# Kernel optimization log

Hardware: AMD Instinct MI355X
Metric: run time of the kernel (lower is better)

The kernel has to match this reference:

```python
import jax, jax.numpy as jnp
import numpy as np
from jax import lax

B, S, D, H, K = 2, 2048, 1024, 16, 3  # batch, seq, embed, heads, conv kernel
DEPTH = D // H


def silu(x):
    return x * jax.nn.sigmoid(x)


def sep_conv1d(x, dw, pw, b):
    """Keras SeparableConv1D, padding='same', activation=silu.
    x: [B,S,C]; dw: [K,1,C] depthwise kernel; pw: [C,F] pointwise; b: [F]."""
    C = x.shape[-1]
    y = lax.conv_general_dilated(
        x, dw, window_strides=(1,), padding='SAME',
        dimension_numbers=('NWC', 'WIO', 'NWC'), feature_group_count=C)
    y = jnp.einsum('bsc,cf->bsf', y, pw) + b
    return silu(y)


def setup_inputs() -> dict:
    key = jax.random.key(0)
    ks = jax.random.split(key, 20)
    sc = 1.0 / np.sqrt(D)
    inp = {
        'v': jax.random.normal(ks[0], (B, S, D), jnp.float32),
        'k': jax.random.normal(ks[1], (B, S, D), jnp.float32),
        'q': jax.random.normal(ks[2], (B, S, D), jnp.float32),
        'mask': jax.random.randint(ks[3], (B, 1, 1, S), 0, 2, jnp.int32),
        # Dense wq/wk/wv (SiLU)
        'wq_w': jax.random.normal(ks[4], (D, D), jnp.float32) * sc,
        'wq_b': jnp.zeros((D,), jnp.float32),
        'wk_w': jax.random.normal(ks[5], (D, D), jnp.float32) * sc,
        'wk_b': jnp.zeros((D,), jnp.float32),
        'wv_w': jax.random.normal(ks[6], (D, D), jnp.float32) * sc,
        'wv_b': jnp.zeros((D,), jnp.float32),
        # SeparableConv1D params (depthwise [K,1,D], pointwise [D,D], bias [D])
        'dwq': jax.random.normal(ks[7], (K, 1, D), jnp.float32) * 0.1,
        'pwq': jax.random.normal(ks[8], (D, D), jnp.float32) * sc,
        'bq': jnp.zeros((D,), jnp.float32),
        'dwk': jax.random.normal(ks[9], (K, 1, D), jnp.float32) * 0.1,
        'pwk': jax.random.normal(ks[10], (D, D), jnp.float32) * sc,
        'bk': jnp.zeros((D,), jnp.float32),
        'dwv': jax.random.normal(ks[11], (K, 1, D), jnp.float32) * 0.1,
        'pwv': jax.random.normal(ks[12], (D, D), jnp.float32) * sc,
        'bv': jnp.zeros((D,), jnp.float32),
        # output Dense (SiLU)
        'wo_w': jax.random.normal(ks[13], (D, D), jnp.float32) * sc,
        'wo_b': jnp.zeros((D,), jnp.float32),
    }
    return inp


def reference(v, k, q, mask, wq_w, wq_b, wk_w, wk_b, wv_w, wv_b,
              dwq, pwq, bq, dwk, pwk, bk, dwv, pwv, bv, wo_w, wo_b):
    # Dense projections with SiLU
    qp = silu(q @ wq_w + wq_b)
    kp = silu(k @ wk_w + wk_b)
    vp = silu(v @ wv_w + wv_b)
    # SeparableConv1D enhancements (SiLU)
    qc = sep_conv1d(qp, dwq, pwq, bq)
    kc = sep_conv1d(kp, dwk, pwk, bk)
    vc = sep_conv1d(vp, dwv, pwv, bv)
    # split heads -> [B,H,S,depth]
    def split(x):
        return x.reshape(B, S, H, DEPTH).transpose(0, 2, 1, 3)
    qh, kh, vh = split(qc), split(kc), split(vc)
    # scaled dot-product attention with additive mask penalty
    logits = jnp.einsum('bhqd,bhkd->bhqk', qh, kh) / jnp.sqrt(jnp.float32(DEPTH))
    logits = logits + mask.astype(jnp.float32) * -1e9
    attn = jax.nn.softmax(logits, axis=-1)
    out = jnp.einsum('bhqk,bhkd->bhqd', attn, vh)
    out = out.transpose(0, 2, 1, 3).reshape(B, S, D)
    return silu(out @ wo_w + wo_b)
```

## Files before the change

kernel.cpp:

```cpp
#include <hip/hip_runtime.h>
#include <hip/hip_fp16.h>
#include <math.h>

#define BB 2
#define SS 2048
#define DD 1024
#define HH 16
#define MTOT (BB*SS)

typedef _Float16 f16;
typedef _Float16 f16x4 __attribute__((ext_vector_type(4)));
typedef _Float16 f16x8 __attribute__((ext_vector_type(8)));
typedef float    f32x4 __attribute__((ext_vector_type(4)));

#define KSCALE 0.1803368801111204f

__device__ __forceinline__ float silu_f(float x) {
    return x / (1.0f + __expf(-x));
}

__device__ __forceinline__ void gload16(void* lds, const void* g) {
    __builtin_amdgcn_global_load_lds(
        (const __attribute__((address_space(1))) unsigned*)g,
        (__attribute__((address_space(3))) unsigned*)lds, 16, 0, 0);
}

__global__ __launch_bounds__(256) void prep(
    const float* __restrict__ q, const float* __restrict__ k, const float* __restrict__ v,
    f16* __restrict__ x0, f16* __restrict__ x1, f16* __restrict__ x2,
    const float* __restrict__ w0, const float* __restrict__ w1, const float* __restrict__ w2,
    const float* __restrict__ w3, const float* __restrict__ w4, const float* __restrict__ w5,
    const float* __restrict__ w6, f16* __restrict__ wt,
    const int* __restrict__ mask, int* __restrict__ uidx, int* __restrict__ ucnt)
{
    __shared__ float ts[64][65];
    const int gid = blockIdx.x;
    const int t = threadIdx.x;

    if (gid < 6144) {
        const int z = gid >> 11;
        const float* src = z == 0 ? q : z == 1 ? k : v;
        f16* dst = z == 0 ? x0 : z == 1 ? x1 : x2;
        const size_t i8 = ((size_t)(gid & 2047) * 256 + t) * 8;
        const float4 a = *(const float4*)(src + i8);
        const float4 b = *(const float4*)(src + i8 + 4);
        f16x8 h = {(f16)a.x,(f16)a.y,(f16)a.z,(f16)a.w,(f16)b.x,(f16)b.y,(f16)b.z,(f16)b.w};
        *(f16x8*)(dst + i8) = h;
    } else if (gid < 7936) {
        const int w = gid - 6144;
        const int z = w >> 8;
        const int rem = w & 255;
        const int bn = (rem & 15) << 6, bk = (rem >> 4) << 6;
        const float* src;
        switch (z) {
            case 0: src = w0; break; case 1: src = w1; break;
            case 2: src = w2; break; case 3: src = w3; break;
            case 4: src = w4; break; case 5: src = w5; break;
            default: src = w6; break;
        }
        f16* dst = wt + ((size_t)z << 20);
        #pragma unroll
        for (int i = 0; i < 4; ++i) {
            const int fid = t + (i << 8);
            const int r = fid >> 4, c4 = (fid & 15) << 2;
            const float4 v4 = *(const float4*)(src + (size_t)(bk + r) * 1024 + bn + c4);
            ts[r][c4 + 0] = v4.x; ts[r][c4 + 1] = v4.y;
            ts[r][c4 + 2] = v4.z; ts[r][c4 + 3] = v4.w;
        }
        __syncthreads();
        #pragma unroll
        for (int i = 0; i < 4; ++i) {
            const int fid = t + (i << 8);
            const int nr = fid >> 4, k4 = (fid & 15) << 2;
            f16x4 h = { (f16)ts[k4 + 0][nr], (f16)ts[k4 + 1][nr],
                        (f16)ts[k4 + 2][nr], (f16)ts[k4 + 3][nr] };
            *(f16x4*)(dst + (size_t)(bn + nr) * 1024 + bk + k4) = h;
        }
    } else {
        int* ps = (int*)ts;
        const int b = gid - 7936;
        int f[8]; int cnt = 0;
        const int base = b * SS + t * 8;
        #pragma unroll
        for (int j = 0; j < 8; ++j) { f[j] = (mask[base + j] == 0); cnt += f[j]; }
        ps[t] = cnt;
        __syncthreads();
        for (int off = 1; off < 256; off <<= 1) {
            const int pv = (t >= off) ? ps[t - off] : 0;
            __syncthreads();
            ps[t] += pv;
            __syncthreads();
        }
        int pos = ps[t] - cnt;
        #pragma unroll
        for (int j = 0; j < 8; ++j)
            if (f[j]) uidx[b * SS + pos++] = t * 8 + j;
        const int total = ps[255];
        const int pad = (total + 63) & ~63;
        for (int j = total + t; j < pad; j += 256) uidx[b * SS + j] = 0;
        if (t == 0) { ucnt[b * 2] = total; ucnt[b * 2 + 1] = pad; }
    }
}

__global__ __launch_bounds__(256) void dwconv3g(
    const f16* __restrict__ p0, const f16* __restrict__ p1, const f16* __restrict__ p2,
    const float* __restrict__ w0, const float* __restrict__ w1, const float* __restrict__ w2,
    f16* __restrict__ o0, f16* __restrict__ o1, f16* __restrict__ o2)
{
    const int z = blockIdx.y;
    const f16* x = z == 0 ? p0 : z == 1 ? p1 : p2;
    const float* dw = z == 0 ? w0 : z == 1 ? w1 : w2;
    f16* y = z == 0 ? o0 : z == 1 ? o1 : o2;
    const size_t i8 = ((size_t)blockIdx.x * 256 + threadIdx.x) * 8;
    const int c = (int)(i8 % DD);
    const int s = (int)((i8 / DD) % SS);
    const f16x8 xc = *(const f16x8*)(x + i8);
    float acc[8];
    #pragma unroll
    for (int j = 0; j < 8; ++j) acc[j] = (float)xc[j] * dw[DD + c + j];
    if (s > 0) {
        const f16x8 xm = *(const f16x8*)(x + i8 - DD);
        #pragma unroll
        for (int j = 0; j < 8; ++j) acc[j] = fmaf((float)xm[j], dw[c + j], acc[j]);
    }
    if (s < SS - 1) {
        const f16x8 xp = *(const f16x8*)(x + i8 + DD);
        #pragma unroll
        for (int j = 0; j < 8; ++j) acc[j] = fmaf((float)xp[j], dw[2 * DD + c + j], acc[j]);
    }
    f16x8 o;
    #pragma unroll
    for (int j = 0; j < 8; ++j) o[j] = (f16)acc[j];
    *(f16x8*)(y + i8) = o;
}

struct GArg { const f16* A; const f16* W; const float* b; void* C; float scale; };

template<int OUTF32>
__global__ __launch_bounds__(256) void gemm_f16(GArg g0, GArg g1, GArg g2)
{
    __shared__ f16 As[128 * 64];
    __shared__ f16 Bs[128 * 64];

    const GArg ga = blockIdx.z == 0 ? g0 : blockIdx.z == 1 ? g1 : g2;
    const int t = threadIdx.x, l = t & 63, wv = t >> 6;
    const int lr = l & 15, lg = l >> 4;
    const int wr = wv >> 1, wc = wv & 1;

    const int bid = blockIdx.y * 8 + blockIdx.x;
    const int sw = (bid & 7) * 32 + (bid >> 3);
    const int brow = (sw >> 3) << 7, bcol = (sw & 7) << 7;

    const int srow = l >> 3;
    const int schk = (l & 7) ^ (l >> 3);
    const f16* Abase = ga.A + (size_t)(brow + wv * 32 + srow) * 1024 + schk * 8;
    const f16* Bbase = ga.W + (size_t)(bcol + wv * 32 + srow) * 1024 + schk * 8;

    f32x4 acc[4][4];
    #pragma unroll
    for (int m = 0; m < 4; ++m)
        #pragma unroll
        for (int n = 0; n < 4; ++n) acc[m][n] = (f32x4){0.f, 0.f, 0.f, 0.f};

    for (int kt = 0; kt < 16; ++kt) {
        const int k0 = kt << 6;
        #pragma unroll
        for (int j = 0; j < 4; ++j) {
            gload16(As + (wv * 4 + j) * 512, Abase + (size_t)j * 8 * 1024 + k0);
            gload16(Bs + (wv * 4 + j) * 512, Bbase + (size_t)j * 8 * 1024 + k0);
        }
        __syncthreads();

        #pragma unroll
        for (int kk = 0; kk < 2; ++kk) {
            f16x8 af[4], bf[4];
            #pragma unroll
            for (int m = 0; m < 4; ++m) {
                const int row = (wr << 6) + (m << 4) + lr;
                const int off = row * 128 + ((((kk << 6) | (lg << 4))) ^ ((lr & 7) << 4));
                af[m] = *(const f16x8*)((const char*)As + off);
            }
            #pragma unroll
            for (int n = 0; n < 4; ++n) {
                const int row = (wc << 6) + (n << 4) + lr;
                const int off = row * 128 + ((((kk << 6) | (lg << 4))) ^ ((lr & 7) << 4));
                bf[n] = *(const f16x8*)((const char*)Bs + off);
            }
            #pragma unroll
            for (int m = 0; m < 4; ++m)
                #pragma unroll
                for (int n = 0; n < 4; ++n)
                    acc[m][n] = __builtin_amdgcn_mfma_f32_16x16x32_f16(af[m], bf[n], acc[m][n], 0, 0, 0);
        }
        __syncthreads();
    }

    float bv[4];
    #pragma unroll
    for (int n = 0; n < 4; ++n) bv[n] = ga.b[bcol + (wc << 6) + (n << 4) + lr];
    #pragma unroll
    for (int m = 0; m < 4; ++m)
        #pragma unroll
        for (int n = 0; n < 4; ++n)
            #pragma unroll
            for (int i = 0; i < 4; ++i) {
                const int row = brow + (wr << 6) + (m << 4) + (lg << 2) + i;
                const int col = bcol + (wc << 6) + (n << 4) + lr;
                const float o = silu_f(acc[m][n][i] + bv[n]) * ga.scale;
                if (OUTF32) ((float*)ga.C)[(size_t)row * 1024 + col] = o;
                else        ((f16*)ga.C)[(size_t)row * 1024 + col] = (f16)o;
            }
}

__global__ __launch_bounds__(512) void attn_f16(
    const f16* __restrict__ Q, const f16* __restrict__ Kf,
    const f16* __restrict__ Vf, const int* __restrict__ uidx,
    const int* __restrict__ ucnt, f16* __restrict__ O)
{
    __shared__ f16 Ks[64 * 64];
    __shared__ f16 Vt[64 * 64];
    __shared__ f16 Pw[8 * 16 * 64];
    __shared__ int uix[2048];

    const int t = threadIdx.x;
    const int l = t & 63, wv = t >> 6;
    const int lr = l & 15, lg = l >> 4;

    const int bid = blockIdx.x;
    const int sw = (bid & 7) * 64 + (bid >> 3);
    const int qb = (sw & 15) << 7;
    const int h  = (sw >> 4) & 15;
    const int b  = sw >> 8;

    const int cnt = ucnt[b * 2];
    const int pad = ucnt[b * 2 + 1];

    const int srow = l >> 3;
    const int schk = (l & 7) ^ (l >> 3);

    const int bkv = (t & 15) << 2;
    const int bnv = (t >> 4) << 2;

    for (int j = t; j < 2048; j += 512) uix[j] = uidx[b * SS + j];

    const size_t qrow = (size_t)b * SS + qb + (wv << 4) + lr;
    const f16x8 aq0 = *(const f16x8*)(Q + qrow * DD + h * 64 + (lg << 3));
    const f16x8 aq1 = *(const f16x8*)(Q + qrow * DD + h * 64 + 32 + (lg << 3));

    float m_i[4], l_i[4];
    f32x4 acc[4];
    #pragma unroll
    for (int i = 0; i < 4; ++i) { m_i[i] = -1e30f; l_i[i] = 0.f; }
    #pragma unroll
    for (int n = 0; n < 4; ++n) acc[n] = (f32x4){0.f, 0.f, 0.f, 0.f};

    const int rdswz = (lr & 7) << 4;
    const size_t bbase = (size_t)b * SS;

    __syncthreads();

    for (int kt = 0; kt < pad; kt += 64) {
        {
            const int krow = uix[kt + wv * 8 + srow];
            gload16(Ks + wv * 512, Kf + (bbase + krow) * DD + h * 64 + schk * 8);
        }
        if (t < 256) {
            f16x4 vl[4];
            #pragma unroll
            for (int r = 0; r < 4; ++r) {
                const int vrow = uix[kt + bkv + r];
                vl[r] = *(const f16x4*)(Vf + (bbase + vrow) * DD + h * 64 + bnv);
            }
            #pragma unroll
            for (int j = 0; j < 4; ++j) {
                f16x4 h4 = { vl[0][j], vl[1][j], vl[2][j], vl[3][j] };
                const int row = bnv + j;
                const int off = row * 128 + ((bkv * 2) ^ ((row & 7) << 4));
                *(f16x4*)((char*)Vt + off) = h4;
            }
        }
        __syncthreads();

        f32x4 s[4];
        const bool full = (kt + 64 <= cnt);
        __builtin_amdgcn_s_setprio(1);
        #pragma unroll
        for (int n = 0; n < 4; ++n) {
            const int row = (n << 4) + lr;
            const f16x8 bk0 = *(const f16x8*)((const char*)Ks + row * 128 + (((lg << 4)) ^ rdswz));
            const f16x8 bk1 = *(const f16x8*)((const char*)Ks + row * 128 + (((64) | (lg << 4)) ^ rdswz));
            f32x4 z = (f32x4){0.f, 0.f, 0.f, 0.f};
            z = __builtin_amdgcn_mfma_f32_16x16x32_f16(aq0, bk0, z, 0, 0, 0);
            z = __builtin_amdgcn_mfma_f32_16x16x32_f16(aq1, bk1, z, 0, 0, 0);
            if (full) {
                #pragma unroll
                for (int i = 0; i < 4; ++i) s[n][i] = z[i];
            } else {
                const bool valid = (kt + row) < cnt;
                #pragma unroll
                for (int i = 0; i < 4; ++i) s[n][i] = valid ? z[i] : -1e30f;
            }
        }
        __builtin_amdgcn_s_setprio(0);

        float pm[4];
        #pragma unroll
        for (int i = 0; i < 4; ++i)
            pm[i] = fmaxf(fmaxf(s[0][i], s[1][i]), fmaxf(s[2][i], s[3][i]));
        #pragma unroll
        for (int i = 0; i < 4; ++i) {
            pm[i] = fmaxf(pm[i], __shfl_xor(pm[i], 1));
            pm[i] = fmaxf(pm[i], __shfl_xor(pm[i], 2));
            pm[i] = fmaxf(pm[i], __shfl_xor(pm[i], 4));
            pm[i] = fmaxf(pm[i], __shfl_xor(pm[i], 8));
        }
        float g = pm[0] - m_i[0];
        #pragma unroll
        for (int i = 1; i < 4; ++i) g = fmaxf(g, pm[i] - m_i[i]);
        if (!__all(g <= 8.0f)) {
            float sc[4];
            #pragma unroll
            for (int i = 0; i < 4; ++i) {
                const float mn = fmaxf(m_i[i], pm[i]);
                sc[i] = exp2f(m_i[i] - mn);
                m_i[i] = mn;
                l_i[i] *= sc[i];
            }
            #pragma unroll
            for (int n = 0; n < 4; ++n)
                #pragma unroll
                for (int i = 0; i < 4; ++i)
                    acc[n][i] *= sc[i];
        }

        #pragma unroll
        for (int n = 0; n < 4; ++n)
            #pragma unroll
            for (int i = 0; i < 4; ++i) {
                const float p = exp2f(s[n][i] - m_i[i]);
                l_i[i] += p;
                const int row = (lg << 2) + i;
                const int off = (wv << 11) + row * 128 + ((((n << 4) + lr) * 2) ^ ((row & 7) << 4));
                *(f16*)((char*)Pw + off) = (f16)p;
            }

        const int poff = (wv << 11) + lr * 128;
        const f16x8 pa0 = *(const f16x8*)((const char*)Pw + poff + (((lg << 4)) ^ rdswz));
        const f16x8 pa1 = *(const f16x8*)((const char*)Pw + poff + (((64) | (lg << 4)) ^ rdswz));
        __builtin_amdgcn_s_setprio(1);
        #pragma unroll
        for (int n = 0; n < 4; ++n) {
            const int row = (n << 4) + lr;
            const f16x8 bv0 = *(const f16x8*)((const char*)Vt + row * 128 + (((lg << 4)) ^ rdswz));
            const f16x8 bv1 = *(const f16x8*)((const char*)Vt + row * 128 + (((64) | (lg << 4)) ^ rdswz));
            acc[n] = __builtin_amdgcn_mfma_f32_16x16x32_f16(pa0, bv0, acc[n], 0, 0, 0);
            acc[n] = __builtin_amdgcn_mfma_f32_16x16x32_f16(pa1, bv1, acc[n], 0, 0, 0);
        }
        __builtin_amdgcn_s_setprio(0);
        __syncthreads();
    }

    #pragma unroll
    for (int i = 0; i < 4; ++i) {
        l_i[i] += __shfl_xor(l_i[i], 1);
        l_i[i] += __shfl_xor(l_i[i], 2);
        l_i[i] += __shfl_xor(l_i[i], 4);
        l_i[i] += __shfl_xor(l_i[i], 8);
    }
    #pragma unroll
    for (int n = 0; n < 4; ++n)
        #pragma unroll
        for (int i = 0; i < 4; ++i) {
            const size_t row = (size_t)b * SS + qb + (wv << 4) + (lg << 2) + i;
            O[row * DD + h * 64 + (n << 4) + lr] = (f16)(acc[n][i] / l_i[i]);
        }
}

extern "C" void kernel_launch(void* const* d_in, const int* in_sizes, int n_in,
                              void* d_out, int out_size, void* d_ws, size_t ws_size,
                              hipStream_t stream) {
    const float* v    = (const float*)d_in[0];
    const float* k    = (const float*)d_in[1];
    const float* q    = (const float*)d_in[2];
    const int*   mask = (const int*)  d_in[3];
    const float* wq_w = (const float*)d_in[4];
    const float* wq_b = (const float*)d_in[5];
    const float* wk_w = (const float*)d_in[6];
    const float* wk_b = (const float*)d_in[7];
    const float* wv_w = (const float*)d_in[8];
    const float* wv_b = (const float*)d_in[9];
    const float* dwq  = (const float*)d_in[10];
    const float* pwq  = (const float*)d_in[11];
    const float* bq   = (const float*)d_in[12];
    const float* dwk  = (const float*)d_in[13];
    const float* pwk  = (const float*)d_in[14];
    const float* bk   = (const float*)d_in[15];
    const float* dwv  = (const float*)d_in[16];
    const float* pwv  = (const float*)d_in[17];
    const float* bv   = (const float*)d_in[18];
    const float* wo_w = (const float*)d_in[19];
    const float* wo_b = (const float*)d_in[20];
    float* out = (float*)d_out;

    const size_t NE = (size_t)MTOT * DD;
    f16* wt = (f16*)d_ws;
    f16* x0 = wt + 7 * (size_t)(1 << 20);
    f16* x1 = x0 + NE;
    f16* x2 = x1 + NE;
    f16* p0 = x2 + NE;
    f16* p1 = p0 + NE;
    f16* p2 = p1 + NE;
    f16* ao = p2 + NE;
    int* uidx = (int*)(ao + NE);
    int* ucnt = uidx + MTOT;

    f16* wtq = wt,              *wtk = wt + (1u<<20), *wtv = wt + 2*(1u<<20);
    f16* wpq = wt + 3*(1u<<20), *wpk = wt + 4*(1u<<20), *wpv = wt + 5*(1u<<20);
    f16* wto = wt + 6*(1u<<20);

    prep<<<dim3(7938), 256, 0, stream>>>(q, k, v, x0, x1, x2,
        wq_w, wk_w, wv_w, pwq, pwk, pwv, wo_w, wt, mask, uidx, ucnt);
    gemm_f16<0><<<dim3(8, 32, 3), 256, 0, stream>>>(
        GArg{x0, wtq, wq_b, p0, 1.0f}, GArg{x1, wtk, wk_b, p1, 1.0f},
        GArg{x2, wtv, wv_b, p2, 1.0f});
    dwconv3g<<<dim3(2048, 3), 256, 0, stream>>>(p0, p1, p2, dwq, dwk, dwv, x0, x1, x2);
    gemm_f16<0><<<dim3(8, 32, 3), 256, 0, stream>>>(
        GArg{x0, wpq, bq, p0, 1.0f}, GArg{x1, wpk, bk, p1, KSCALE},
        GArg{x2, wpv, bv, p2, 1.0f});
    attn_f16<<<dim3(512), 512, 0, stream>>>(p0, p1, p2, uidx, ucnt, ao);
    gemm_f16<1><<<dim3(8, 32, 1), 256, 0, stream>>>(
        GArg{ao, wto, wo_b, out, 1.0f}, GArg{ao, wto, wo_b, out, 1.0f},
        GArg{ao, wto, wo_b, out, 1.0f});
}
```

Before: 201.6 us.

## Process two query tiles per attention block to reuse K/V tiles

Each attention block now handles 256 query rows as two independent 128-row sets that share the same K/V tiles loaded into LDS. The grid shrinks from 512 to 256 blocks, which halves global K/V gather traffic and the number of barriers per query row. The row-max shuffle reduction now runs only when a rescale is triggered, and the trigger test uses each lane's partial max. The cost is higher register pressure from double accumulators, and one block per CU leaves less overlap between blocks.

```diff
diff --git a/kernel.cpp b/kernel.cpp
--- a/kernel.cpp
+++ b/kernel.cpp
@@ -227,10 +227,10 @@
     const int lr = l & 15, lg = l >> 4;
 
     const int bid = blockIdx.x;
-    const int sw = (bid & 7) * 64 + (bid >> 3);
-    const int qb = (sw & 15) << 7;
-    const int h  = (sw >> 4) & 15;
-    const int b  = sw >> 8;
+    const int sw = (bid & 7) * 32 + (bid >> 3);
+    const int qb = (sw & 7) << 8;
+    const int h  = (sw >> 3) & 15;
+    const int b  = sw >> 7;
 
     const int cnt = ucnt[b * 2];
     const int pad = ucnt[b * 2 + 1];
@@ -243,21 +243,96 @@
 
     for (int j = t; j < 2048; j += 512) uix[j] = uidx[b * SS + j];
 
-    const size_t qrow = (size_t)b * SS + qb + (wv << 4) + lr;
-    const f16x8 aq0 = *(const f16x8*)(Q + qrow * DD + h * 64 + (lg << 3));
-    const f16x8 aq1 = *(const f16x8*)(Q + qrow * DD + h * 64 + 32 + (lg << 3));
-
-    float m_i[4], l_i[4];
-    f32x4 acc[4];
-    #pragma unroll
-    for (int i = 0; i < 4; ++i) { m_i[i] = -1e30f; l_i[i] = 0.f; }
-    #pragma unroll
-    for (int n = 0; n < 4; ++n) acc[n] = (f32x4){0.f, 0.f, 0.f, 0.f};
+    const size_t bbase = (size_t)b * SS;
+    const size_t qrowA = bbase + qb + (wv << 4) + lr;
+    const size_t qrowB = qrowA + 128;
+    const f16x8 aqA0 = *(const f16x8*)(Q + qrowA * DD + h * 64 + (lg << 3));
+    const f16x8 aqA1 = *(const f16x8*)(Q + qrowA * DD + h * 64 + 32 + (lg << 3));
+    const f16x8 aqB0 = *(const f16x8*)(Q + qrowB * DD + h * 64 + (lg << 3));
+    const f16x8 aqB1 = *(const f16x8*)(Q + qrowB * DD + h * 64 + 32 + (lg << 3));
+
+    float mA[4], lA[4], mB[4], lB[4];
+    f32x4 accA[4], accB[4];
+    #pragma unroll
+    for (int i = 0; i < 4; ++i) { mA[i] = -1e30f; lA[i] = 0.f; mB[i] = -1e30f; lB[i] = 0.f; }
+    #pragma unroll
+    for (int n = 0; n < 4; ++n) { accA[n] = (f32x4){0.f,0.f,0.f,0.f}; accB[n] = (f32x4){0.f,0.f,0.f,0.f}; }
 
     const int rdswz = (lr & 7) << 4;
-    const size_t bbase = (size_t)b * SS;
+    const int poff = (wv << 11) + lr * 128;
 
     __syncthreads();
+
+#define PROCESS(AQ0, AQ1, M_, L_, ACC_) do {                                  \
+    f32x4 s[4];                                                               \
+    __builtin_amdgcn_s_setprio(1);                                            \
+    _Pragma("unroll")                                                         \
+    for (int n = 0; n < 4; ++n) {                                             \
+        f32x4 z = (f32x4){0.f, 0.f, 0.f, 0.f};                                \
+        z = __builtin_amdgcn_mfma_f32_16x16x32_f16(AQ0, bk0[n], z, 0, 0, 0);  \
+        z = __builtin_amdgcn_mfma_f32_16x16x32_f16(AQ1, bk1[n], z, 0, 0, 0);  \
+        if (full) {                                                           \
+            _Pragma("unroll")                                                 \
+            for (int i = 0; i < 4; ++i) s[n][i] = z[i];                       \
+        } else {                                                              \
+            const bool valid = (kt + (n << 4) + lr) < cnt;                    \
+            _Pragma("unroll")                                                 \
+            for (int i = 0; i < 4; ++i) s[n][i] = valid ? z[i] : -1e30f;      \
+        }                                                                     \
+    }                                                                         \
+    __builtin_amdgcn_s_setprio(0);                                            \
+    float pm[4];                                                              \
+    _Pragma("unroll")                                                         \
+    for (int i = 0; i < 4; ++i)                                               \
+        pm[i] = fmaxf(fmaxf(s[0][i], s[1][i]), fmaxf(s[2][i], s[3][i]));      \
+    float g = pm[0] - M_[0];                                                  \
+    _Pragma("unroll")                                                         \
+    for (int i = 1; i < 4; ++i) g = fmaxf(g, pm[i] - M_[i]);                  \
+    if (!__all(g <= 8.0f)) {                 \
+        float sc[4];                                                          \
+        _Pragma("unroll")                                                     \
+        for (int i = 0; i < 4; ++i) {                                         \
+            float pr = pm[i];                                                 \
+            pr = fmaxf(pr, __shfl_xor(pr, 1));                                \
+            pr = fmaxf(pr, __shfl_xor(pr, 2));                                \
+            pr = fmaxf(pr, __shfl_xor(pr, 4));                                \
+            pr = fmaxf(pr, __shfl_xor(pr, 8));                                \
+            const float mn = fmaxf(M_[i], pr);                                \
+            sc[i] = exp2f(M_[i] - mn);                                        \
+            M_[i] = mn;                                                       \
+            L_[i] *= sc[i];                                                   \
+        }                                                                     \
+        _Pragma("unroll")                                                     \
+        for (int n = 0; n < 4; ++n)                                           \
+            _Pragma("unroll")                                                 \
+            for (int i = 0; i < 4; ++i) ACC_[n][i] *= sc[i];                  \
+    }                                                                         \
+    _Pragma("unroll")                                                         \
+    for (int n = 0; n < 4; ++n)                                               \
+        _Pragma("unroll")                                                     \
+        for (int i = 0; i < 4; ++i) {                                         \
+            const float p = exp2f(s[n][i] - M_[i]);       \
+            L_[i] += p;                                                       \
+            const int row = (lg << 2) + i;                                    \
+            const int off = (wv << 11) + row * 128 +                          \
+                            ((((n << 4) + lr) * 2) ^ ((row & 7) << 4));       \
+            *(f16*)((char*)Pw + off) = (f16)p;                                \
+        }                                                                     \
+    {                                                                         \
+        const f16x8 pa0 = *(const f16x8*)((const char*)Pw + poff + (((lg << 4)) ^ rdswz));        \
+        const f16x8 pa1 = *(const f16x8*)((const char*)Pw + poff + (((64) | (lg << 4)) ^ rdswz)); \
+        __builtin_amdgcn_s_setprio(1);                                        \
+        _Pragma("unroll")                                                     \
+        for (int n = 0; n < 4; ++n) {                                         \
+            const int row = (n << 4) + lr;                                    \
+            const f16x8 bv0 = *(const f16x8*)((const char*)Vt + row * 128 + (((lg << 4)) ^ rdswz));        \
+            const f16x8 bv1 = *(const f16x8*)((const char*)Vt + row * 128 + (((64) | (lg << 4)) ^ rdswz)); \
+            ACC_[n] = __builtin_amdgcn_mfma_f32_16x16x32_f16(pa0, bv0, ACC_[n], 0, 0, 0);  \
+            ACC_[n] = __builtin_amdgcn_mfma_f32_16x16x32_f16(pa1, bv1, ACC_[n], 0, 0, 0);  \
+        }                                                                     \
+        __builtin_amdgcn_s_setprio(0);                                        \
+    }                                                                         \
+} while (0)
 
     for (int kt = 0; kt < pad; kt += 64) {
         {
@@ -281,98 +356,40 @@
         }
         __syncthreads();
 
-        f32x4 s[4];
-        const bool full = (kt + 64 <= cnt);
-        __builtin_amdgcn_s_setprio(1);
+        f16x8 bk0[4], bk1[4];
         #pragma unroll
         for (int n = 0; n < 4; ++n) {
             const int row = (n << 4) + lr;
-            const f16x8 bk0 = *(const f16x8*)((const char*)Ks + row * 128 + (((lg << 4)) ^ rdswz));
-            const f16x8 bk1 = *(const f16x8*)((const char*)Ks + row * 128 + (((64) | (lg << 4)) ^ rdswz));
-            f32x4 z = (f32x4){0.f, 0.f, 0.f, 0.f};
-            z = __builtin_amdgcn_mfma_f32_16x16x32_f16(aq0, bk0, z, 0, 0, 0);
-            z = __builtin_amdgcn_mfma_f32_16x16x32_f16(aq1, bk1, z, 0, 0, 0);
-            if (full) {
-                #pragma unroll
-                for (int i = 0; i < 4; ++i) s[n][i] = z[i];
-            } else {
-                const bool valid = (kt + row) < cnt;
-                #pragma unroll
-                for (int i = 0; i < 4; ++i) s[n][i] = valid ? z[i] : -1e30f;
-            }
-        }
-        __builtin_amdgcn_s_setprio(0);
-
-        float pm[4];
-        #pragma unroll
-        for (int i = 0; i < 4; ++i)
-            pm[i] = fmaxf(fmaxf(s[0][i], s[1][i]), fmaxf(s[2][i], s[3][i]));
+            bk0[n] = *(const f16x8*)((const char*)Ks + row * 128 + (((lg << 4)) ^ rdswz));
+            bk1[n] = *(const f16x8*)((const char*)Ks + row * 128 + (((64) | (lg << 4)) ^ rdswz));
+        }
+        const bool full = (kt + 64 <= cnt);
+
+        PROCESS(aqA0, aqA1, mA, lA, accA);
+        PROCESS(aqB0, aqB1, mB, lB, accB);
+
+        __syncthreads();
+    }
+#undef PROCESS
+
+    #pragma unroll
+    for (int i = 0; i < 4; ++i) {
+        lA[i] += __shfl_xor(lA[i], 1);
+        lA[i] += __shfl_xor(lA[i], 2);
+        lA[i] += __shfl_xor(lA[i], 4);
+        lA[i] += __shfl_xor(lA[i], 8);
+        lB[i] += __shfl_xor(lB[i], 1);
+        lB[i] += __shfl_xor(lB[i], 2);
+        lB[i] += __shfl_xor(lB[i], 4);
+        lB[i] += __shfl_xor(lB[i], 8);
+    }
+    #pragma unroll
+    for (int n = 0; n < 4; ++n)
         #pragma unroll
         for (int i = 0; i < 4; ++i) {
-            pm[i] = fmaxf(pm[i], __shfl_xor(pm[i], 1));
-            pm[i] = fmaxf(pm[i], __shfl_xor(pm[i], 2));
-            pm[i] = fmaxf(pm[i], __shfl_xor(pm[i], 4));
-            pm[i] = fmaxf(pm[i], __shfl_xor(pm[i], 8));
-        }
-        float g = pm[0] - m_i[0];
-        #pragma unroll
-        for (int i = 1; i < 4; ++i) g = fmaxf(g, pm[i] - m_i[i]);
-        if (!__all(g <= 8.0f)) {
-            float sc[4];
-            #pragma unroll
-            for (int i = 0; i < 4; ++i) {
-                const float mn = fmaxf(m_i[i], pm[i]);
-                sc[i] = exp2f(m_i[i] - mn);
-                m_i[i] = mn;
-                l_i[i] *= sc[i];
-            }
-            #pragma unroll
-            for (int n = 0; n < 4; ++n)
-                #pragma unroll
-                for (int i = 0; i < 4; ++i)
-                    acc[n][i] *= sc[i];
-        }
-
-        #pragma unroll
-        for (int n = 0; n < 4; ++n)
-            #pragma unroll
-            for (int i = 0; i < 4; ++i) {
-                const float p = exp2f(s[n][i] - m_i[i]);
-                l_i[i] += p;
-                const int row = (lg << 2) + i;
-                const int off = (wv << 11) + row * 128 + ((((n << 4) + lr) * 2) ^ ((row & 7) << 4));
-                *(f16*)((char*)Pw + off) = (f16)p;
-            }
-
-        const int poff = (wv << 11) + lr * 128;
-        const f16x8 pa0 = *(const f16x8*)((const char*)Pw + poff + (((lg << 4)) ^ rdswz));
-        const f16x8 pa1 = *(const f16x8*)((const char*)Pw + poff + (((64) | (lg << 4)) ^ rdswz));
-        __builtin_amdgcn_s_setprio(1);
-        #pragma unroll
-        for (int n = 0; n < 4; ++n) {
-            const int row = (n << 4) + lr;
-            const f16x8 bv0 = *(const f16x8*)((const char*)Vt + row * 128 + (((lg << 4)) ^ rdswz));
-            const f16x8 bv1 = *(const f16x8*)((const char*)Vt + row * 128 + (((64) | (lg << 4)) ^ rdswz));
-            acc[n] = __builtin_amdgcn_mfma_f32_16x16x32_f16(pa0, bv0, acc[n], 0, 0, 0);
-            acc[n] = __builtin_amdgcn_mfma_f32_16x16x32_f16(pa1, bv1, acc[n], 0, 0, 0);
-        }
-        __builtin_amdgcn_s_setprio(0);
-        __syncthreads();
-    }
-
-    #pragma unroll
-    for (int i = 0; i < 4; ++i) {
-        l_i[i] += __shfl_xor(l_i[i], 1);
-        l_i[i] += __shfl_xor(l_i[i], 2);
-        l_i[i] += __shfl_xor(l_i[i], 4);
-        l_i[i] += __shfl_xor(l_i[i], 8);
-    }
-    #pragma unroll
-    for (int n = 0; n < 4; ++n)
-        #pragma unroll
-        for (int i = 0; i < 4; ++i) {
-            const size_t row = (size_t)b * SS + qb + (wv << 4) + (lg << 2) + i;
-            O[row * DD + h * 64 + (n << 4) + lr] = (f16)(acc[n][i] / l_i[i]);
+            const size_t rowA = bbase + qb + (wv << 4) + (lg << 2) + i;
+            O[rowA * DD + h * 64 + (n << 4) + lr] = (f16)(accA[n][i] / lA[i]);
+            O[(rowA + 128) * DD + h * 64 + (n << 4) + lr] = (f16)(accB[n][i] / lB[i]);
         }
 }
 
@@ -427,7 +444,7 @@
     gemm_f16<0><<<dim3(8, 32, 3), 256, 0, stream>>>(
         GArg{x0, wpq, bq, p0, 1.0f}, GArg{x1, wpk, bk, p1, KSCALE},
         GArg{x2, wpv, bv, p2, 1.0f});
-    attn_f16<<<dim3(512), 512, 0, stream>>>(p0, p1, p2, uidx, ucnt, ao);
+    attn_f16<<<dim3(256), 512, 0, stream>>>(p0, p1, p2, uidx, ucnt, ao);
     gemm_f16<1><<<dim3(8, 32, 1), 256, 0, stream>>>(
         GArg{ao, wto, wo_b, out, 1.0f}, GArg{ao, wto, wo_b, out, 1.0f},
         GArg{ao, wto, wo_b, out, 1.0f});
```

Result: no change. 203.4 us (+0.9%).
